# Kernel tuning notes

Hardware: AMD Instinct MI355X
Metric: run time of the kernel (lower is better)

Reference implementation:

```python
import jax, jax.numpy as jnp
import numpy as np

F_DIM = 256; H = 4; LAT = 256; BOT = 128
B = 64; NPG = 180; N = B * NPG; E = N * 16; HF = H * F_DIM
NEG_SLOPE = 0.2  # PyG GATConv default LeakyReLU slope


def _gat(x, src, dst, W, att_s, att_d, bias):
    # PyG GATConv (concat=True): h = x W, per-edge score LeakyReLU(a_s[src]+a_d[dst]),
    # softmax over incoming edges of each dst, weighted sum, concat heads, + bias.
    h = (x @ W).reshape(N, H, F_DIM)
    a_s = jnp.einsum('nhc,hc->nh', h, att_s)
    a_d = jnp.einsum('nhc,hc->nh', h, att_d)
    e = jax.nn.leaky_relu(a_s[src] + a_d[dst], NEG_SLOPE)          # [E+N, H]
    m = jax.ops.segment_max(e, dst, num_segments=N)                # stable softmax per dst
    p = jnp.exp(e - m[dst])
    s = jax.ops.segment_sum(p, dst, num_segments=N)
    alpha = p / (s[dst] + 1e-16)
    out = jax.ops.segment_sum(alpha[:, :, None] * h[src], dst, num_segments=N)
    return out.reshape(N, HF) + bias


def setup_inputs() -> dict:
    key = jax.random.key(0)
    ks = jax.random.split(key, 40)
    def rn(i, shape, scale):
        return jax.random.normal(ks[i], shape, jnp.float32) * jnp.float32(scale)
    inp = {}
    inp['z'] = jax.random.normal(ks[0], (B, LAT), jnp.float32)
    inp['condition'] = jax.random.normal(ks[1], (B, BOT), jnp.float32)
    dst = jax.random.randint(ks[2], (E,), 0, N)
    off = jax.random.randint(ks[3], (E,), 1, NPG)
    src = (dst + off) % N  # no self-loops by construction (PyG adds them itself)
    inp['edge_index'] = jnp.stack([src, dst]).astype(jnp.int32)
    inp['batch'] = jnp.repeat(jnp.arange(B, dtype=jnp.int32), NPG)
    def lin(i, fin, fout):
        s = 1.0 / np.sqrt(fin)
        return rn(i, (fin, fout), s), rn(i + 1, (fout,), s)
    inp['W_init'], inp['b_init'] = lin(4, LAT + BOT, F_DIM)
    inp['W1'] = rn(6, (F_DIM + 180, HF), 1.0 / np.sqrt(F_DIM + 180))
    inp['as1'] = rn(7, (H, F_DIM), 0.1); inp['ad1'] = rn(8, (H, F_DIM), 0.1)
    inp['b1'] = rn(9, (HF,), 0.1)
    inp['W2'] = rn(10, (HF, HF), 1.0 / np.sqrt(HF))
    inp['as2'] = rn(11, (H, F_DIM), 0.1); inp['ad2'] = rn(12, (H, F_DIM), 0.1)
    inp['b2'] = rn(13, (HF,), 0.1)
    inp['W3'] = rn(14, (HF, HF), 1.0 / np.sqrt(HF))
    inp['as3'] = rn(15, (H, F_DIM), 0.1); inp['ad3'] = rn(16, (H, F_DIM), 0.1)
    inp['b3'] = rn(17, (HF,), 0.1)
    inp['Wp'], inp['bp'] = lin(18, HF, F_DIM)
    inp['Wfp'], inp['bfp'] = lin(20, F_DIM, 2)
    inp['Ws'], inp['bs'] = lin(22, HF, F_DIM)
    inp['Wfs'], inp['bfs'] = lin(24, F_DIM, 2)
    inp['Wt'], inp['bt'] = lin(26, HF, F_DIM)
    inp['Wft'], inp['bft'] = lin(28, F_DIM, 1)
    return inp


def reference(z, condition, edge_index, batch, W_init, b_init,
              W1, as1, ad1, b1, W2, as2, ad2, b2, W3, as3, ad3, b3,
              Wp, bp, Wfp, bfp, Ws, bs, Wfs, bfs, Wt, bt, Wft, bft):
    zc = jnp.concatenate([z, condition], axis=1) @ W_init + b_init  # [B, F]
    x = zc[batch]                                                    # [N, F]
    # node order within each (sorted) batch segment -> one-hot(180)
    start = jnp.searchsorted(batch, jnp.arange(B, dtype=batch.dtype))
    order = jnp.arange(N) - start[batch]
    pos = jax.nn.one_hot(order, 180, dtype=x.dtype)
    x = jax.nn.relu(jnp.concatenate([x, pos], axis=1))               # [N, F+180]
    # add self loops (PyG GATConv default add_self_loops=True)
    loops = jnp.arange(N, dtype=edge_index.dtype)
    src = jnp.concatenate([edge_index[0], loops])
    dst = jnp.concatenate([edge_index[1], loops])
    x = jax.nn.relu(_gat(x, src, dst, W1, as1, ad1, b1))
    x = jax.nn.relu(_gat(x, src, dst, W2, as2, ad2, b2))
    x = jax.nn.relu(_gat(x, src, dst, W3, as3, ad3, b3))
    out_pos = jax.nn.relu(x @ Wp + bp) @ Wfp + bfp     # [N, 2]
    out_size = jax.nn.relu(x @ Ws + bs) @ Wfs + bfs    # [N, 2]
    out_theta = jax.nn.relu(x @ Wt + bt) @ Wft + bft   # [N, 1]
    return out_pos, out_size, out_theta
```

## Files before the change

kernel.cpp:

```cpp
#include <hip/hip_runtime.h>
#include <hip/hip_bf16.h>

#define NODES 11520
#define EDGES 184320
#define NB    64
#define NPG   180
#define CAP   64

typedef __bf16 bf16x8 __attribute__((ext_vector_type(8)));
typedef __bf16 bf16x4 __attribute__((ext_vector_type(4)));
typedef float  f32x4  __attribute__((ext_vector_type(4)));

__global__ __launch_bounds__(256) void k_init(
    const float* __restrict__ z, const float* __restrict__ cond,
    const float* __restrict__ Wi, const float* __restrict__ bi,
    const float* __restrict__ W1, float* __restrict__ Y1)
{
    __shared__ float xr[384];
    __shared__ float part[4][256];
    __shared__ float zr[256];
    const int b = blockIdx.x, t = threadIdx.x;
    xr[t] = (t < 256) ? z[b * 256 + t] : 0.f;
    if (t < 128) xr[256 + t] = cond[b * 128 + t];
    __syncthreads();
    {
        const int kq = t >> 6, tc = t & 63;
        f32x4 acc = {0.f, 0.f, 0.f, 0.f};
        const float* wbase = Wi + (size_t)(kq * 96) * 256 + 4 * tc;
        const float* xb = xr + kq * 96;
#pragma unroll 8
        for (int k = 0; k < 96; ++k) {
            const float4 w = *(const float4*)(wbase + (size_t)k * 256);
            const float x = xb[k];
            acc[0] = fmaf(x, w.x, acc[0]);
            acc[1] = fmaf(x, w.y, acc[1]);
            acc[2] = fmaf(x, w.z, acc[2]);
            acc[3] = fmaf(x, w.w, acc[3]);
        }
        *(f32x4*)&part[kq][4 * tc] = acc;
    }
    __syncthreads();
    zr[t] = fmaxf(bi[t] + part[0][t] + part[1][t] + part[2][t] + part[3][t], 0.f);
    __syncthreads();
    {
        f32x4 acc = {0.f, 0.f, 0.f, 0.f};
#pragma unroll 8
        for (int k = 0; k < 256; ++k) {
            const float4 w = *(const float4*)(W1 + (size_t)k * 1024 + 4 * t);
            const float x = zr[k];
            acc[0] = fmaf(x, w.x, acc[0]);
            acc[1] = fmaf(x, w.y, acc[1]);
            acc[2] = fmaf(x, w.z, acc[2]);
            acc[3] = fmaf(x, w.w, acc[3]);
        }
        *(f32x4*)(Y1 + (size_t)b * 1024 + 4 * t) = acc;
    }
}

__global__ __launch_bounds__(256) void k_h1(
    const float* __restrict__ Y1, const float* __restrict__ W1,
    const float* __restrict__ atts, const float* __restrict__ attd,
    __bf16* __restrict__ hb, float* __restrict__ asb, float* __restrict__ adb)
{
    const int n = blockIdx.x, t = threadIdx.x;
    const int g = n / NPG, o = n - g * NPG;
    const float4 y = *(const float4*)(Y1 + (size_t)g * 1024 + 4 * t);
    const float4 w = *(const float4*)(W1 + (size_t)(256 + o) * 1024 + 4 * t);
    const float4 h = {y.x + w.x, y.y + w.y, y.z + w.z, y.w + w.w};
    bf16x4 hv = {(__bf16)h.x, (__bf16)h.y, (__bf16)h.z, (__bf16)h.w};
    *(bf16x4*)(hb + (size_t)n * 1024 + 4 * t) = hv;
    const int head = t >> 6, c0 = (t & 63) * 4;
    const float4 s4 = *(const float4*)(atts + head * 256 + c0);
    const float4 d4 = *(const float4*)(attd + head * 256 + c0);
    float ps = h.x * s4.x + h.y * s4.y + h.z * s4.z + h.w * s4.w;
    float pd = h.x * d4.x + h.y * d4.y + h.z * d4.z + h.w * d4.w;
    for (int off = 32; off; off >>= 1) {
        ps += __shfl_xor(ps, off, 64);
        pd += __shfl_xor(pd, off, 64);
    }
    if ((t & 63) == 0) { asb[n * 4 + head] = ps; adb[n * 4 + head] = pd; }
}

__global__ __launch_bounds__(256) void k_hist(
    const int* __restrict__ ei, int* __restrict__ counts,
    int* __restrict__ bucket)
{
    const int e = blockIdx.x * 256 + threadIdx.x;
    if (e >= EDGES) return;
    const int s = ei[e], d = ei[EDGES + e];
    const int pos = atomicAdd(&counts[d], 1);
    if (pos < CAP) bucket[(size_t)d * CAP + pos] = s;
}

__global__ __launch_bounds__(256) void k_agg(
    const __bf16* __restrict__ hb, const float* __restrict__ asb,
    const float* __restrict__ adb, const int* __restrict__ counts,
    const int* __restrict__ bucket, const float* __restrict__ bias,
    __bf16* __restrict__ xout)
{
    const int l = blockIdx.x;
    const int n = (l & 7) * (NODES / 8) + (l >> 3);
    const int t = threadIdx.x;
    __shared__ float sc[CAP + 1][4];
    __shared__ int   ssrc[CAP + 1];
    __shared__ float sinv[4];
    const int deg = min(counts[n], CAP);
    const int ne  = deg + 1;
    if (t < deg)       ssrc[t] = bucket[(size_t)n * CAP + t];
    else if (t == deg) ssrc[t] = n;
    __syncthreads();
    if (t < ne) {
        const int s = ssrc[t];
        const float4 as4 = *(const float4*)(asb + (size_t)s * 4);
        const float4 ad4 = *(const float4*)(adb + (size_t)n * 4);
        const float v0 = as4.x + ad4.x, v1 = as4.y + ad4.y;
        const float v2 = as4.z + ad4.z, v3 = as4.w + ad4.w;
        sc[t][0] = v0 > 0.f ? v0 : 0.2f * v0;
        sc[t][1] = v1 > 0.f ? v1 : 0.2f * v1;
        sc[t][2] = v2 > 0.f ? v2 : 0.2f * v2;
        sc[t][3] = v3 > 0.f ? v3 : 0.2f * v3;
    }
    __syncthreads();
    const int wv = t >> 6, ln = t & 63;
    {
        float m = -1e30f;
        for (int k = ln; k < ne; k += 64) m = fmaxf(m, sc[k][wv]);
        for (int off = 32; off; off >>= 1) m = fmaxf(m, __shfl_xor(m, off, 64));
        float s = 0.f;
        for (int k = ln; k < ne; k += 64) {
            const float p = __expf(sc[k][wv] - m);
            sc[k][wv] = p;
            s += p;
        }
        for (int off = 32; off; off >>= 1) s += __shfl_xor(s, off, 64);
        if (ln == 0) sinv[wv] = 1.f / (s + 1e-16f);
    }
    __syncthreads();
    const int j0 = t * 4;
    const float inv = sinv[wv];
    float a0 = 0, a1 = 0, a2 = 0, a3 = 0;
    int k = 0;
    for (; k + 4 <= ne; k += 4) {
        float al[4]; bf16x4 hv[4];
#pragma unroll
        for (int u = 0; u < 4; ++u) {
            al[u] = sc[k + u][wv] * inv;
            hv[u] = *(const bf16x4*)(hb + (size_t)ssrc[k + u] * 1024 + j0);
        }
#pragma unroll
        for (int u = 0; u < 4; ++u) {
            a0 = fmaf(al[u], (float)hv[u][0], a0);
            a1 = fmaf(al[u], (float)hv[u][1], a1);
            a2 = fmaf(al[u], (float)hv[u][2], a2);
            a3 = fmaf(al[u], (float)hv[u][3], a3);
        }
    }
    for (; k < ne; ++k) {
        const float al = sc[k][wv] * inv;
        const bf16x4 hv = *(const bf16x4*)(hb + (size_t)ssrc[k] * 1024 + j0);
        a0 = fmaf(al, (float)hv[0], a0);
        a1 = fmaf(al, (float)hv[1], a1);
        a2 = fmaf(al, (float)hv[2], a2);
        a3 = fmaf(al, (float)hv[3], a3);
    }
    const float4 b4 = *(const float4*)(bias + j0);
    bf16x4 o = {(__bf16)fmaxf(a0 + b4.x, 0.f), (__bf16)fmaxf(a1 + b4.y, 0.f),
                (__bf16)fmaxf(a2 + b4.z, 0.f), (__bf16)fmaxf(a3 + b4.w, 0.f)};
    *(bf16x4*)(xout + (size_t)n * 1024 + j0) = o;
}

__global__ __launch_bounds__(256) void k_transW(
    const float* __restrict__ W2, const float* __restrict__ W3,
    __bf16* __restrict__ W2t, __bf16* __restrict__ W3t)
{
    const float* W = blockIdx.z ? W3 : W2;
    __bf16* WT = blockIdx.z ? W3t : W2t;
    __shared__ float t[32][33];
    const int n0 = blockIdx.x * 32, k0 = blockIdx.y * 32;
    const int tx = threadIdx.x & 31, ty = threadIdx.x >> 5;
#pragma unroll
    for (int i = 0; i < 32; i += 8)
        t[ty + i][tx] = W[(size_t)(k0 + ty + i) * 1024 + n0 + tx];
    __syncthreads();
#pragma unroll
    for (int i = 0; i < 32; i += 8)
        WT[(size_t)(n0 + ty + i) * 1024 + k0 + tx] = (__bf16)t[tx][ty + i];
}

__global__ __launch_bounds__(256) void k_transH(
    const float* __restrict__ Wp, const float* __restrict__ Ws,
    const float* __restrict__ Wt, __bf16* __restrict__ WHt,
    const float* __restrict__ bp, const float* __restrict__ bs,
    const float* __restrict__ bt, float* __restrict__ bc)
{
    if (blockIdx.x == 8) {
        if (blockIdx.y == 0) {
            const int t = blockIdx.z * 256 + threadIdx.x;
            const float v = blockIdx.z == 0 ? bp[threadIdx.x]
                          : blockIdx.z == 1 ? bs[threadIdx.x] : bt[threadIdx.x];
            bc[t] = v;
        }
        return;
    }
    const float* W = blockIdx.z == 0 ? Wp : blockIdx.z == 1 ? Ws : Wt;
    __bf16* WT = WHt + (size_t)blockIdx.z * 256 * 1024;
    __shared__ float t[32][33];
    const int n0 = blockIdx.x * 32, k0 = blockIdx.y * 32;
    const int tx = threadIdx.x & 31, ty = threadIdx.x >> 5;
#pragma unroll
    for (int i = 0; i < 32; i += 8)
        t[ty + i][tx] = W[(size_t)(k0 + ty + i) * 256 + n0 + tx];
    __syncthreads();
#pragma unroll
    for (int i = 0; i < 32; i += 8)
        WT[(size_t)(n0 + ty + i) * 1024 + k0 + tx] = (__bf16)t[tx][ty + i];
}

__global__ __launch_bounds__(256) void gemm_bf16_h(
    const __bf16* __restrict__ A,
    const __bf16* __restrict__ BT,
    __bf16* __restrict__ Cb,
    const float* __restrict__ atts, const float* __restrict__ attd,
    float* __restrict__ asb, float* __restrict__ adb,
    int M, int N, int K)
{
    const int lb = blockIdx.x;
    const int g = lb & 7, idx = lb >> 3;
    const int bx = idx & 7;
    const int by = (idx >> 3) * 8 + g;
    if (by * 128 >= M) return;
    const int m0 = by * 128, n0 = bx * 128;

    __shared__ __bf16 As[2 * 128 * 32];
    __shared__ __bf16 Bs[2 * 128 * 32];
    const int tid = threadIdx.x;
    const int w = tid >> 6, l = tid & 63;
    const int lr = l >> 2;
    const int lk = (l & 3) * 8;
    const int quad = l >> 4, r16 = l & 15;
    const int wm = (w >> 1) * 64, wn = (w & 1) * 64;

    f32x4 acc[4][4];
#pragma unroll
    for (int i = 0; i < 4; ++i)
#pragma unroll
        for (int j = 0; j < 4; ++j)
            acc[i][j] = (f32x4){0.f, 0.f, 0.f, 0.f};

    for (int k0 = 0; k0 < K; k0 += 64) {
#pragma unroll
        for (int h = 0; h < 2; ++h) {
#pragma unroll
            for (int cc = 0; cc < 2; ++cc) {
                const int c = 2 * w + cc;
                const int row = c * 16 + lr;
                __builtin_amdgcn_global_load_lds(
                    (const __attribute__((address_space(1))) void*)
                        (A + (size_t)(m0 + row) * K + k0 + h * 32 + lk),
                    (__attribute__((address_space(3))) void*)
                        (As + h * 4096 + c * 512),
                    16, 0, 0);
                __builtin_amdgcn_global_load_lds(
                    (const __attribute__((address_space(1))) void*)
                        (BT + (size_t)(n0 + row) * K + k0 + h * 32 + lk),
                    (__attribute__((address_space(3))) void*)
                        (Bs + h * 4096 + c * 512),
                    16, 0, 0);
            }
        }
        __syncthreads();
#pragma unroll
        for (int h = 0; h < 2; ++h) {
            bf16x8 af[4], bfr[4];
#pragma unroll
            for (int i = 0; i < 4; ++i)
                af[i] = *(const bf16x8*)(As + h * 4096 +
                                         (wm + i * 16 + r16) * 32 + quad * 8);
#pragma unroll
            for (int j = 0; j < 4; ++j)
                bfr[j] = *(const bf16x8*)(Bs + h * 4096 +
                                          (wn + j * 16 + r16) * 32 + quad * 8);
#pragma unroll
            for (int i = 0; i < 4; ++i)
#pragma unroll
                for (int j = 0; j < 4; ++j)
                    acc[i][j] = __builtin_amdgcn_mfma_f32_16x16x32_bf16(
                        af[i], bfr[j], acc[i][j], 0, 0, 0);
        }
        __syncthreads();
    }
    const int head = (n0 + wn) >> 8;
    const float* Sa = atts + head * 256;
    const float* Da = attd + head * 256;
#pragma unroll
    for (int i = 0; i < 4; ++i) {
#pragma unroll
        for (int r = 0; r < 4; ++r) {
            const int mg = m0 + wm + i * 16 + quad * 4 + r;
            float ps = 0.f, pd = 0.f;
#pragma unroll
            for (int j = 0; j < 4; ++j) {
                const int ng = n0 + wn + j * 16 + r16;
                const float v = acc[i][j][r];
                const int cl = ng & 255;
                ps = fmaf(v, Sa[cl], ps);
                pd = fmaf(v, Da[cl], pd);
                Cb[(size_t)mg * N + ng] = (__bf16)v;
            }
            for (int off = 8; off; off >>= 1) {
                ps += __shfl_xor(ps, off, 64);
                pd += __shfl_xor(pd, off, 64);
            }
            if (r16 == 0) {
                atomicAdd(&asb[mg * 4 + head], ps);
                atomicAdd(&adb[mg * 4 + head], pd);
            }
        }
    }
}

__global__ __launch_bounds__(256) void gemm_bf16_f32(
    const __bf16* __restrict__ A, const __bf16* __restrict__ BT,
    float* __restrict__ C, const float* __restrict__ bias,
    int M, int N, int K)
{
    const int lb = blockIdx.x;
    const int g = lb & 7, idx = lb >> 3;
    const int bx = idx % 6;
    const int by = (idx / 6) * 8 + g;
    if (by * 128 >= M) return;
    const int m0 = by * 128, n0 = bx * 128;

    __shared__ __bf16 As[2 * 128 * 32];
    __shared__ __bf16 Bs[2 * 128 * 32];
    const int tid = threadIdx.x;
    const int w = tid >> 6, l = tid & 63;
    const int lr = l >> 2;
    const int lk = (l & 3) * 8;
    const int quad = l >> 4, r16 = l & 15;
    const int wm = (w >> 1) * 64, wn = (w & 1) * 64;

    f32x4 acc[4][4];
#pragma unroll
    for (int i = 0; i < 4; ++i)
#pragma unroll
        for (int j = 0; j < 4; ++j)
            acc[i][j] = (f32x4){0.f, 0.f, 0.f, 0.f};

    for (int k0 = 0; k0 < K; k0 += 64) {
#pragma unroll
        for (int h = 0; h < 2; ++h) {
#pragma unroll
            for (int cc = 0; cc < 2; ++cc) {
                const int c = 2 * w + cc;
                const int row = c * 16 + lr;
                __builtin_amdgcn_global_load_lds(
                    (const __attribute__((address_space(1))) void*)
                        (A + (size_t)(m0 + row) * K + k0 + h * 32 + lk),
                    (__attribute__((address_space(3))) void*)
                        (As + h * 4096 + c * 512),
                    16, 0, 0);
                __builtin_amdgcn_global_load_lds(
                    (const __attribute__((address_space(1))) void*)
                        (BT + (size_t)(n0 + row) * K + k0 + h * 32 + lk),
                    (__attribute__((address_space(3))) void*)
                        (Bs + h * 4096 + c * 512),
                    16, 0, 0);
            }
        }
        __syncthreads();
#pragma unroll
        for (int h = 0; h < 2; ++h) {
            bf16x8 af[4], bfr[4];
#pragma unroll
            for (int i = 0; i < 4; ++i)
                af[i] = *(const bf16x8*)(As + h * 4096 +
                                         (wm + i * 16 + r16) * 32 + quad * 8);
#pragma unroll
            for (int j = 0; j < 4; ++j)
                bfr[j] = *(const bf16x8*)(Bs + h * 4096 +
                                          (wn + j * 16 + r16) * 32 + quad * 8);
#pragma unroll
            for (int i = 0; i < 4; ++i)
#pragma unroll
                for (int j = 0; j < 4; ++j)
                    acc[i][j] = __builtin_amdgcn_mfma_f32_16x16x32_bf16(
                        af[i], bfr[j], acc[i][j], 0, 0, 0);
        }
        __syncthreads();
    }
#pragma unroll
    for (int i = 0; i < 4; ++i) {
        const int mg = m0 + wm + i * 16 + quad * 4;
#pragma unroll
        for (int j = 0; j < 4; ++j) {
            const int ng = n0 + wn + j * 16 + r16;
            const float bz = bias[ng];
#pragma unroll
            for (int r = 0; r < 4; ++r)
                C[(size_t)(mg + r) * N + ng] = fmaxf(acc[i][j][r] + bz, 0.f);
        }
    }
}

__global__ __launch_bounds__(320) void k_final(
    const float* __restrict__ T,
    const float* __restrict__ Wfp, const float* __restrict__ bfp,
    const float* __restrict__ Wfs, const float* __restrict__ bfs,
    const float* __restrict__ Wft, const float* __restrict__ bft,
    float* __restrict__ out)
{
    const int n = blockIdx.x;
    const int w = threadIdx.x >> 6, l = threadIdx.x & 63;
    const float* trow;
    const float* Wf;
    float bv;
    int col, stride, oidx;
    if (w < 2) {
        trow = T + (size_t)n * 768;       Wf = Wfp; bv = bfp[w];
        col = w; stride = 2; oidx = 2 * n + w;
    } else if (w < 4) {
        trow = T + (size_t)n * 768 + 256; Wf = Wfs; bv = bfs[w - 2];
        col = w - 2; stride = 2; oidx = 2 * NODES + 2 * n + (w - 2);
    } else {
        trow = T + (size_t)n * 768 + 512; Wf = Wft; bv = bft[0];
        col = 0; stride = 1; oidx = 4 * NODES + n;
    }
    float s = 0.f;
    for (int c = l; c < 256; c += 64) s = fmaf(trow[c], Wf[c * stride + col], s);
    for (int off = 32; off; off >>= 1) s += __shfl_xor(s, off, 64);
    if (l == 0) out[oidx] = s + bv;
}

extern "C" void kernel_launch(void* const* d_in, const int* in_sizes, int n_in,
                              void* d_out, int out_size, void* d_ws, size_t ws_size,
                              hipStream_t stream)
{
    const float* z    = (const float*)d_in[0];
    const float* cond = (const float*)d_in[1];
    const int*   ei   = (const int*)  d_in[2];
    const float* Wi   = (const float*)d_in[4];
    const float* bi   = (const float*)d_in[5];
    const float* W1   = (const float*)d_in[6];
    const float* as1  = (const float*)d_in[7];
    const float* ad1  = (const float*)d_in[8];
    const float* b1   = (const float*)d_in[9];
    const float* W2   = (const float*)d_in[10];
    const float* as2  = (const float*)d_in[11];
    const float* ad2  = (const float*)d_in[12];
    const float* b2   = (const float*)d_in[13];
    const float* W3   = (const float*)d_in[14];
    const float* as3  = (const float*)d_in[15];
    const float* ad3  = (const float*)d_in[16];
    const float* b3   = (const float*)d_in[17];
    const float* Wp   = (const float*)d_in[18];
    const float* bp   = (const float*)d_in[19];
    const float* Wfp  = (const float*)d_in[20];
    const float* bfp  = (const float*)d_in[21];
    const float* Ws   = (const float*)d_in[22];
    const float* bs   = (const float*)d_in[23];
    const float* Wfs  = (const float*)d_in[24];
    const float* bfs  = (const float*)d_in[25];
    const float* Wt   = (const float*)d_in[26];
    const float* bt   = (const float*)d_in[27];
    const float* Wft  = (const float*)d_in[28];
    const float* bft  = (const float*)d_in[29];
    float* out = (float*)d_out;

    char* p = (char*)d_ws;
    __bf16* hb    = (__bf16*)p;           p += (size_t)NODES * 1024 * 2;
    __bf16* xb16  = (__bf16*)p;           p += (size_t)NODES * 1024 * 2;
    float* Tbuf   = (float*)p;            p += (size_t)NODES * 768 * 4;
    float* asb    = (float*)p;            p += (size_t)NODES * 4 * 4;
    float* adb    = (float*)p;            p += (size_t)NODES * 4 * 4;
    float* Y1     = (float*)p;            p += 64 * 1024 * 4;
    int*   counts = (int*)p;              p += (size_t)NODES * 4;
    int*   bucket = (int*)p;              p += (size_t)NODES * CAP * 4;
    __bf16* W2t   = (__bf16*)p;           p += (size_t)1024 * 1024 * 2;
    __bf16* W3t   = (__bf16*)p;           p += (size_t)1024 * 1024 * 2;
    __bf16* WHt   = (__bf16*)p;           p += (size_t)768 * 1024 * 2;
    float* biascat= (float*)p;            p += 768 * 4;

    k_transW<<<dim3(32, 32, 2), 256, 0, stream>>>(W2, W3, W2t, W3t);
    k_transH<<<dim3(9, 32, 3), 256, 0, stream>>>(Wp, Ws, Wt, WHt,
                                                 bp, bs, bt, biascat);

    hipMemsetAsync(counts, 0, NODES * sizeof(int), stream);
    k_hist<<<EDGES / 256, 256, 0, stream>>>(ei, counts, bucket);

    k_init<<<NB, 256, 0, stream>>>(z, cond, Wi, bi, W1, Y1);
    k_h1<<<NODES, 256, 0, stream>>>(Y1, W1, as1, ad1, hb, asb, adb);
    k_agg<<<NODES, 256, 0, stream>>>(hb, asb, adb, counts, bucket, b1, xb16);

    hipMemsetAsync(asb, 0, (size_t)NODES * 8 * sizeof(float), stream);
    gemm_bf16_h<<<8 * 96, 256, 0, stream>>>(xb16, W2t, hb, as2, ad2,
                                            asb, adb, NODES, 1024, 1024);
    k_agg<<<NODES, 256, 0, stream>>>(hb, asb, adb, counts, bucket, b2, xb16);

    hipMemsetAsync(asb, 0, (size_t)NODES * 8 * sizeof(float), stream);
    gemm_bf16_h<<<8 * 96, 256, 0, stream>>>(xb16, W3t, hb, as3, ad3,
                                            asb, adb, NODES, 1024, 1024);
    k_agg<<<NODES, 256, 0, stream>>>(hb, asb, adb, counts, bucket, b3, xb16);

    gemm_bf16_f32<<<6 * 96, 256, 0, stream>>>(xb16, WHt, Tbuf, biascat,
                                              NODES, 768, 1024);
    k_final<<<NODES, 320, 0, stream>>>(Tbuf, Wfp, bfp, Wfs, bfs, Wft, bft, out);
}
```

Before: 445.3 us.

## Double-buffer GEMM, fuse head MLP epilogue, pack two nodes per agg block

```diff
diff --git a/kernel.cpp b/kernel.cpp
--- a/kernel.cpp
+++ b/kernel.cpp
@@ -60,9 +60,12 @@
 __global__ __launch_bounds__(256) void k_h1(
     const float* __restrict__ Y1, const float* __restrict__ W1,
     const float* __restrict__ atts, const float* __restrict__ attd,
-    __bf16* __restrict__ hb, float* __restrict__ asb, float* __restrict__ adb)
+    __bf16* __restrict__ hb, float* __restrict__ asb, float* __restrict__ adb,
+    float* __restrict__ zas, float* __restrict__ zad)
 {
     const int n = blockIdx.x, t = threadIdx.x;
+    if (t < 4)      zas[n * 4 + t] = 0.f;
+    else if (t < 8) zad[n * 4 + (t - 4)] = 0.f;
     const int g = n / NPG, o = n - g * NPG;
     const float4 y = *(const float4*)(Y1 + (size_t)g * 1024 + 4 * t);
     const float4 w = *(const float4*)(W1 + (size_t)(256 + o) * 1024 + 4 * t);
@@ -96,77 +99,90 @@
     const __bf16* __restrict__ hb, const float* __restrict__ asb,
     const float* __restrict__ adb, const int* __restrict__ counts,
     const int* __restrict__ bucket, const float* __restrict__ bias,
-    __bf16* __restrict__ xout)
-{
-    const int l = blockIdx.x;
-    const int n = (l & 7) * (NODES / 8) + (l >> 3);
+    __bf16* __restrict__ xout, float* __restrict__ zas, float* __restrict__ zad)
+{
+    const int b = blockIdx.x;
+    const int nb = (b & 7) * (NODES / 8) + 2 * (b >> 3);
     const int t = threadIdx.x;
-    __shared__ float sc[CAP + 1][4];
-    __shared__ int   ssrc[CAP + 1];
-    __shared__ float sinv[4];
+    const int half = t >> 7, tt = t & 127;
+    const int n = nb + half;
+    __shared__ float sc[2][CAP + 1][4];
+    __shared__ int   ssrc[2][CAP + 1];
+    __shared__ float sinv[2][4];
+    if (zas != nullptr) {
+        if (t < 8)       zas[nb * 4 + t] = 0.f;
+        else if (t < 16) zad[nb * 4 + (t - 8)] = 0.f;
+    }
     const int deg = min(counts[n], CAP);
     const int ne  = deg + 1;
-    if (t < deg)       ssrc[t] = bucket[(size_t)n * CAP + t];
-    else if (t == deg) ssrc[t] = n;
-    __syncthreads();
-    if (t < ne) {
-        const int s = ssrc[t];
+    if (tt < deg)       ssrc[half][tt] = bucket[(size_t)n * CAP + tt];
+    else if (tt == deg) ssrc[half][tt] = n;
+    __syncthreads();
+    if (tt < ne) {
+        const int s = ssrc[half][tt];
         const float4 as4 = *(const float4*)(asb + (size_t)s * 4);
         const float4 ad4 = *(const float4*)(adb + (size_t)n * 4);
         const float v0 = as4.x + ad4.x, v1 = as4.y + ad4.y;
         const float v2 = as4.z + ad4.z, v3 = as4.w + ad4.w;
-        sc[t][0] = v0 > 0.f ? v0 : 0.2f * v0;
-        sc[t][1] = v1 > 0.f ? v1 : 0.2f * v1;
-        sc[t][2] = v2 > 0.f ? v2 : 0.2f * v2;
-        sc[t][3] = v3 > 0.f ? v3 : 0.2f * v3;
-    }
-    __syncthreads();
-    const int wv = t >> 6, ln = t & 63;
-    {
+        sc[half][tt][0] = v0 > 0.f ? v0 : 0.2f * v0;
+        sc[half][tt][1] = v1 > 0.f ? v1 : 0.2f * v1;
+        sc[half][tt][2] = v2 > 0.f ? v2 : 0.2f * v2;
+        sc[half][tt][3] = v3 > 0.f ? v3 : 0.2f * v3;
+    }
+    __syncthreads();
+    const int ln = t & 63, hw = (t >> 6) & 1;
+#pragma unroll
+    for (int hh = 0; hh < 2; ++hh) {
+        const int head = hw * 2 + hh;
         float m = -1e30f;
-        for (int k = ln; k < ne; k += 64) m = fmaxf(m, sc[k][wv]);
+        for (int k = ln; k < ne; k += 64) m = fmaxf(m, sc[half][k][head]);
         for (int off = 32; off; off >>= 1) m = fmaxf(m, __shfl_xor(m, off, 64));
         float s = 0.f;
         for (int k = ln; k < ne; k += 64) {
-            const float p = __expf(sc[k][wv] - m);
-            sc[k][wv] = p;
+            const float p = __expf(sc[half][k][head] - m);
+            sc[half][k][head] = p;
             s += p;
         }
         for (int off = 32; off; off >>= 1) s += __shfl_xor(s, off, 64);
-        if (ln == 0) sinv[wv] = 1.f / (s + 1e-16f);
-    }
-    __syncthreads();
-    const int j0 = t * 4;
-    const float inv = sinv[wv];
-    float a0 = 0, a1 = 0, a2 = 0, a3 = 0;
+        if (ln == 0) sinv[half][head] = 1.f / (s + 1e-16f);
+    }
+    __syncthreads();
+    const int j0 = tt * 8, hd = tt >> 5;
+    const float inv = sinv[half][hd];
+    float a[8] = {0, 0, 0, 0, 0, 0, 0, 0};
     int k = 0;
     for (; k + 4 <= ne; k += 4) {
-        float al[4]; bf16x4 hv[4];
+        float al[4]; bf16x8 hv[4];
 #pragma unroll
         for (int u = 0; u < 4; ++u) {
-            al[u] = sc[k + u][wv] * inv;
-            hv[u] = *(const bf16x4*)(hb + (size_t)ssrc[k + u] * 1024 + j0);
-        }
-#pragma unroll
-        for (int u = 0; u < 4; ++u) {
-            a0 = fmaf(al[u], (float)hv[u][0], a0);
-            a1 = fmaf(al[u], (float)hv[u][1], a1);
-            a2 = fmaf(al[u], (float)hv[u][2], a2);
-            a3 = fmaf(al[u], (float)hv[u][3], a3);
-        }
+            al[u] = sc[half][k + u][hd] * inv;
+            hv[u] = *(const bf16x8*)(hb + (size_t)ssrc[half][k + u] * 1024 + j0);
+        }
+#pragma unroll
+        for (int u = 0; u < 4; ++u)
+#pragma unroll
+            for (int e = 0; e < 8; ++e)
+                a[e] = fmaf(al[u], (float)hv[u][e], a[e]);
     }
     for (; k < ne; ++k) {
-        const float al = sc[k][wv] * inv;
-        const bf16x4 hv = *(const bf16x4*)(hb + (size_t)ssrc[k] * 1024 + j0);
-        a0 = fmaf(al, (float)hv[0], a0);
-        a1 = fmaf(al, (float)hv[1], a1);
-        a2 = fmaf(al, (float)hv[2], a2);
-        a3 = fmaf(al, (float)hv[3], a3);
-    }
-    const float4 b4 = *(const float4*)(bias + j0);
-    bf16x4 o = {(__bf16)fmaxf(a0 + b4.x, 0.f), (__bf16)fmaxf(a1 + b4.y, 0.f),
-                (__bf16)fmaxf(a2 + b4.z, 0.f), (__bf16)fmaxf(a3 + b4.w, 0.f)};
-    *(bf16x4*)(xout + (size_t)n * 1024 + j0) = o;
+        const float al = sc[half][k][hd] * inv;
+        const bf16x8 hv = *(const bf16x8*)(hb + (size_t)ssrc[half][k] * 1024 + j0);
+#pragma unroll
+        for (int e = 0; e < 8; ++e)
+            a[e] = fmaf(al, (float)hv[e], a[e]);
+    }
+    const float4 b4a = *(const float4*)(bias + j0);
+    const float4 b4b = *(const float4*)(bias + j0 + 4);
+    bf16x8 o;
+    o[0] = (__bf16)fmaxf(a[0] + b4a.x, 0.f);
+    o[1] = (__bf16)fmaxf(a[1] + b4a.y, 0.f);
+    o[2] = (__bf16)fmaxf(a[2] + b4a.z, 0.f);
+    o[3] = (__bf16)fmaxf(a[3] + b4a.w, 0.f);
+    o[4] = (__bf16)fmaxf(a[4] + b4b.x, 0.f);
+    o[5] = (__bf16)fmaxf(a[5] + b4b.y, 0.f);
+    o[6] = (__bf16)fmaxf(a[6] + b4b.z, 0.f);
+    o[7] = (__bf16)fmaxf(a[7] + b4b.w, 0.f);
+    *(bf16x8*)(xout + (size_t)n * 1024 + j0) = o;
 }
 
 __global__ __launch_bounds__(256) void k_transW(
@@ -216,9 +232,70 @@
         WT[(size_t)(n0 + ty + i) * 1024 + k0 + tx] = (__bf16)t[tx][ty + i];
 }
 
+#define STAGE(buf, kbase)                                                      \
+    {                                                                          \
+        _Pragma("unroll")                                                      \
+        for (int h = 0; h < 2; ++h) {                                          \
+            _Pragma("unroll")                                                  \
+            for (int cc = 0; cc < 2; ++cc) {                                   \
+                const int c = 2 * w + cc;                                      \
+                const int row = c * 16 + lr;                                   \
+                __builtin_amdgcn_global_load_lds(                              \
+                    (const __attribute__((address_space(1))) void*)            \
+                        (A + (size_t)(m0 + row) * K + (kbase) + h * 32 + lk),  \
+                    (__attribute__((address_space(3))) void*)                  \
+                        (As + (buf) * 8192 + h * 4096 + c * 512), 16, 0, 0);   \
+                __builtin_amdgcn_global_load_lds(                              \
+                    (const __attribute__((address_space(1))) void*)            \
+                        (BT + (size_t)(n0 + row) * K + (kbase) + h * 32 + lk), \
+                    (__attribute__((address_space(3))) void*)                  \
+                        (Bs + (buf) * 8192 + h * 4096 + c * 512), 16, 0, 0);   \
+            }                                                                  \
+        }                                                                      \
+    }
+
+#define COMPUTE(buf)                                                           \
+    {                                                                          \
+        _Pragma("unroll")                                                      \
+        for (int h = 0; h < 2; ++h) {                                          \
+            bf16x8 af[4], bfr[4];                                              \
+            _Pragma("unroll")                                                  \
+            for (int i = 0; i < 4; ++i)                                        \
+                af[i] = *(const bf16x8*)(As + (buf) * 8192 + h * 4096 +        \
+                                         (wm + i * 16 + r16) * 32 + quad * 8); \
+            _Pragma("unroll")                                                  \
+            for (int j = 0; j < 4; ++j)                                        \
+                bfr[j] = *(const bf16x8*)(Bs + (buf) * 8192 + h * 4096 +       \
+                                          (wn + j * 16 + r16) * 32 + quad * 8);\
+            _Pragma("unroll")                                                  \
+            for (int i = 0; i < 4; ++i)                                        \
+                _Pragma("unroll")                                              \
+                for (int j = 0; j < 4; ++j)                                    \
+                    acc[i][j] = __builtin_amdgcn_mfma_f32_16x16x32_bf16(       \
+                        af[i], bfr[j], acc[i][j], 0, 0, 0);                    \
+        }                                                                      \
+    }
+
+#define GEMM_MAINLOOP()                                                        \
+    f32x4 acc[4][4];                                                           \
+    _Pragma("unroll")                                                          \
+    for (int i = 0; i < 4; ++i)                                                \
+        _Pragma("unroll")                                                      \
+        for (int j = 0; j < 4; ++j)                                            \
+            acc[i][j] = (f32x4){0.f, 0.f, 0.f, 0.f};                           \
+    STAGE(0, 0);                                                               \
+    int cur = 0;                                                               \
+    for (int k0 = 64; k0 < K; k0 += 64) {                                      \
+        __syncthreads();                                                       \
+        STAGE(cur ^ 1, k0);                                                    \
+        COMPUTE(cur);                                                          \
+        cur ^= 1;                                                              \
+    }                                                                          \
+    __syncthreads();                                                           \
+    COMPUTE(cur);
+
 __global__ __launch_bounds__(256) void gemm_bf16_h(
-    const __bf16* __restrict__ A,
-    const __bf16* __restrict__ BT,
+    const __bf16* __restrict__ A, const __bf16* __restrict__ BT,
     __bf16* __restrict__ Cb,
     const float* __restrict__ atts, const float* __restrict__ attd,
     float* __restrict__ asb, float* __restrict__ adb,
@@ -231,67 +308,24 @@
     if (by * 128 >= M) return;
     const int m0 = by * 128, n0 = bx * 128;
 
-    __shared__ __bf16 As[2 * 128 * 32];
-    __shared__ __bf16 Bs[2 * 128 * 32];
+    __shared__ __bf16 As[2 * 128 * 64];
+    __shared__ __bf16 Bs[2 * 128 * 64];
     const int tid = threadIdx.x;
     const int w = tid >> 6, l = tid & 63;
-    const int lr = l >> 2;
-    const int lk = (l & 3) * 8;
+    const int lr = l >> 2, lk = (l & 3) * 8;
     const int quad = l >> 4, r16 = l & 15;
     const int wm = (w >> 1) * 64, wn = (w & 1) * 64;
 
-    f32x4 acc[4][4];
-#pragma unroll
-    for (int i = 0; i < 4; ++i)
-#pragma unroll
-        for (int j = 0; j < 4; ++j)
-            acc[i][j] = (f32x4){0.f, 0.f, 0.f, 0.f};
-
-    for (int k0 = 0; k0 < K; k0 += 64) {
-#pragma unroll
-        for (int h = 0; h < 2; ++h) {
-#pragma unroll
-            for (int cc = 0; cc < 2; ++cc) {
-                const int c = 2 * w + cc;
-                const int row = c * 16 + lr;
-                __builtin_amdgcn_global_load_lds(
-                    (const __attribute__((address_space(1))) void*)
-                        (A + (size_t)(m0 + row) * K + k0 + h * 32 + lk),
-                    (__attribute__((address_space(3))) void*)
-                        (As + h * 4096 + c * 512),
-                    16, 0, 0);
-                __builtin_amdgcn_global_load_lds(
-                    (const __attribute__((address_space(1))) void*)
-                        (BT + (size_t)(n0 + row) * K + k0 + h * 32 + lk),
-                    (__attribute__((address_space(3))) void*)
-                        (Bs + h * 4096 + c * 512),
-                    16, 0, 0);
-            }
-        }
-        __syncthreads();
-#pragma unroll
-        for (int h = 0; h < 2; ++h) {
-            bf16x8 af[4], bfr[4];
-#pragma unroll
-            for (int i = 0; i < 4; ++i)
-                af[i] = *(const bf16x8*)(As + h * 4096 +
-                                         (wm + i * 16 + r16) * 32 + quad * 8);
-#pragma unroll
-            for (int j = 0; j < 4; ++j)
-                bfr[j] = *(const bf16x8*)(Bs + h * 4096 +
-                                          (wn + j * 16 + r16) * 32 + quad * 8);
-#pragma unroll
-            for (int i = 0; i < 4; ++i)
-#pragma unroll
-                for (int j = 0; j < 4; ++j)
-                    acc[i][j] = __builtin_amdgcn_mfma_f32_16x16x32_bf16(
-                        af[i], bfr[j], acc[i][j], 0, 0, 0);
-        }
-        __syncthreads();
-    }
+    GEMM_MAINLOOP();
+
     const int head = (n0 + wn) >> 8;
-    const float* Sa = atts + head * 256;
-    const float* Da = attd + head * 256;
+    float sa[4], da[4];
+#pragma unroll
+    for (int j = 0; j < 4; ++j) {
+        const int cl = (n0 + wn + j * 16 + r16) & 255;
+        sa[j] = atts[head * 256 + cl];
+        da[j] = attd[head * 256 + cl];
+    }
 #pragma unroll
     for (int i = 0; i < 4; ++i) {
 #pragma unroll
@@ -302,9 +336,8 @@
             for (int j = 0; j < 4; ++j) {
                 const int ng = n0 + wn + j * 16 + r16;
                 const float v = acc[i][j][r];
-                const int cl = ng & 255;
-                ps = fmaf(v, Sa[cl], ps);
-                pd = fmaf(v, Da[cl], pd);
+                ps = fmaf(v, sa[j], ps);
+                pd = fmaf(v, da[j], pd);
                 Cb[(size_t)mg * N + ng] = (__bf16)v;
             }
             for (int off = 8; off; off >>= 1) {
@@ -319,10 +352,13 @@
     }
 }
 
-__global__ __launch_bounds__(256) void gemm_bf16_f32(
+__global__ __launch_bounds__(256) void gemm_heads(
     const __bf16* __restrict__ A, const __bf16* __restrict__ BT,
-    float* __restrict__ C, const float* __restrict__ bias,
-    int M, int N, int K)
+    const float* __restrict__ biascat,
+    const float* __restrict__ Wfp, const float* __restrict__ bfp,
+    const float* __restrict__ Wfs, const float* __restrict__ bfs,
+    const float* __restrict__ Wft, const float* __restrict__ bft,
+    float* __restrict__ out, int M, int K)
 {
     const int lb = blockIdx.x;
     const int g = lb & 7, idx = lb >> 3;
@@ -331,105 +367,57 @@
     if (by * 128 >= M) return;
     const int m0 = by * 128, n0 = bx * 128;
 
-    __shared__ __bf16 As[2 * 128 * 32];
-    __shared__ __bf16 Bs[2 * 128 * 32];
+    __shared__ __bf16 As[2 * 128 * 64];
+    __shared__ __bf16 Bs[2 * 128 * 64];
     const int tid = threadIdx.x;
     const int w = tid >> 6, l = tid & 63;
-    const int lr = l >> 2;
-    const int lk = (l & 3) * 8;
+    const int lr = l >> 2, lk = (l & 3) * 8;
     const int quad = l >> 4, r16 = l & 15;
     const int wm = (w >> 1) * 64, wn = (w & 1) * 64;
 
-    f32x4 acc[4][4];
-#pragma unroll
-    for (int i = 0; i < 4; ++i)
-#pragma unroll
-        for (int j = 0; j < 4; ++j)
-            acc[i][j] = (f32x4){0.f, 0.f, 0.f, 0.f};
-
-    for (int k0 = 0; k0 < K; k0 += 64) {
-#pragma unroll
-        for (int h = 0; h < 2; ++h) {
-#pragma unroll
-            for (int cc = 0; cc < 2; ++cc) {
-                const int c = 2 * w + cc;
-                const int row = c * 16 + lr;
-                __builtin_amdgcn_global_load_lds(
-                    (const __attribute__((address_space(1))) void*)
-                        (A + (size_t)(m0 + row) * K + k0 + h * 32 + lk),
-                    (__attribute__((address_space(3))) void*)
-                        (As + h * 4096 + c * 512),
-                    16, 0, 0);
-                __builtin_amdgcn_global_load_lds(
-                    (const __attribute__((address_space(1))) void*)
-                        (BT + (size_t)(n0 + row) * K + k0 + h * 32 + lk),
-                    (__attribute__((address_space(3))) void*)
-                        (Bs + h * 4096 + c * 512),
-                    16, 0, 0);
-            }
-        }
-        __syncthreads();
-#pragma unroll
-        for (int h = 0; h < 2; ++h) {
-            bf16x8 af[4], bfr[4];
-#pragma unroll
-            for (int i = 0; i < 4; ++i)
-                af[i] = *(const bf16x8*)(As + h * 4096 +
-                                         (wm + i * 16 + r16) * 32 + quad * 8);
-#pragma unroll
-            for (int j = 0; j < 4; ++j)
-                bfr[j] = *(const bf16x8*)(Bs + h * 4096 +
-                                          (wn + j * 16 + r16) * 32 + quad * 8);
-#pragma unroll
-            for (int i = 0; i < 4; ++i)
-#pragma unroll
-                for (int j = 0; j < 4; ++j)
-                    acc[i][j] = __builtin_amdgcn_mfma_f32_16x16x32_bf16(
-                        af[i], bfr[j], acc[i][j], 0, 0, 0);
-        }
-        __syncthreads();
-    }
+    GEMM_MAINLOOP();
+
+    const int hg = bx >> 1;
+    const float* Wf = hg == 0 ? Wfp : hg == 1 ? Wfs : Wft;
+    const int nout = hg == 2 ? 1 : 2;
+    float wf0[4], wf1[4], bz[4];
+#pragma unroll
+    for (int j = 0; j < 4; ++j) {
+        const int ng = n0 + wn + j * 16 + r16;
+        const int cl = ng & 255;
+        bz[j]  = biascat[ng];
+        wf0[j] = Wf[cl * nout];
+        wf1[j] = nout == 2 ? Wf[cl * nout + 1] : 0.f;
+    }
+    const bool addb = ((bx & 1) == 0) && (wn == 0);
+    const float fb0 = hg == 0 ? bfp[0] : hg == 1 ? bfs[0] : bft[0];
+    const float fb1 = hg == 2 ? 0.f : (hg == 0 ? bfp[1] : bfs[1]);
 #pragma unroll
     for (int i = 0; i < 4; ++i) {
-        const int mg = m0 + wm + i * 16 + quad * 4;
-#pragma unroll
-        for (int j = 0; j < 4; ++j) {
-            const int ng = n0 + wn + j * 16 + r16;
-            const float bz = bias[ng];
-#pragma unroll
-            for (int r = 0; r < 4; ++r)
-                C[(size_t)(mg + r) * N + ng] = fmaxf(acc[i][j][r] + bz, 0.f);
-        }
-    }
-}
-
-__global__ __launch_bounds__(320) void k_final(
-    const float* __restrict__ T,
-    const float* __restrict__ Wfp, const float* __restrict__ bfp,
-    const float* __restrict__ Wfs, const float* __restrict__ bfs,
-    const float* __restrict__ Wft, const float* __restrict__ bft,
-    float* __restrict__ out)
-{
-    const int n = blockIdx.x;
-    const int w = threadIdx.x >> 6, l = threadIdx.x & 63;
-    const float* trow;
-    const float* Wf;
-    float bv;
-    int col, stride, oidx;
-    if (w < 2) {
-        trow = T + (size_t)n * 768;       Wf = Wfp; bv = bfp[w];
-        col = w; stride = 2; oidx = 2 * n + w;
-    } else if (w < 4) {
-        trow = T + (size_t)n * 768 + 256; Wf = Wfs; bv = bfs[w - 2];
-        col = w - 2; stride = 2; oidx = 2 * NODES + 2 * n + (w - 2);
-    } else {
-        trow = T + (size_t)n * 768 + 512; Wf = Wft; bv = bft[0];
-        col = 0; stride = 1; oidx = 4 * NODES + n;
-    }
-    float s = 0.f;
-    for (int c = l; c < 256; c += 64) s = fmaf(trow[c], Wf[c * stride + col], s);
-    for (int off = 32; off; off >>= 1) s += __shfl_xor(s, off, 64);
-    if (l == 0) out[oidx] = s + bv;
+#pragma unroll
+        for (int r = 0; r < 4; ++r) {
+            const int mg = m0 + wm + i * 16 + quad * 4 + r;
+            float o0 = 0.f, o1 = 0.f;
+#pragma unroll
+            for (int j = 0; j < 4; ++j) {
+                const float v = fmaxf(acc[i][j][r] + bz[j], 0.f);
+                o0 = fmaf(v, wf0[j], o0);
+                o1 = fmaf(v, wf1[j], o1);
+            }
+            for (int off = 8; off; off >>= 1) {
+                o0 += __shfl_xor(o0, off, 64);
+                o1 += __shfl_xor(o1, off, 64);
+            }
+            if (r16 == 0) {
+                if (addb) { o0 += fb0; o1 += fb1; }
+                const size_t base = hg == 0 ? 2 * (size_t)mg
+                                 : hg == 1 ? 2 * (size_t)NODES + 2 * (size_t)mg
+                                 : 4 * (size_t)NODES + (size_t)mg;
+                atomicAdd(&out[base], o0);
+                if (nout == 2) atomicAdd(&out[base + 1], o1);
+            }
+        }
+    }
 }
 
 extern "C" void kernel_launch(void* const* d_in, const int* in_sizes, int n_in,
@@ -470,9 +458,10 @@
     char* p = (char*)d_ws;
     __bf16* hb    = (__bf16*)p;           p += (size_t)NODES * 1024 * 2;
     __bf16* xb16  = (__bf16*)p;           p += (size_t)NODES * 1024 * 2;
-    float* Tbuf   = (float*)p;            p += (size_t)NODES * 768 * 4;
-    float* asb    = (float*)p;            p += (size_t)NODES * 4 * 4;
-    float* adb    = (float*)p;            p += (size_t)NODES * 4 * 4;
+    float* asA    = (float*)p;            p += (size_t)NODES * 4 * 4;
+    float* adA    = (float*)p;            p += (size_t)NODES * 4 * 4;
+    float* asB    = (float*)p;            p += (size_t)NODES * 4 * 4;
+    float* adB    = (float*)p;            p += (size_t)NODES * 4 * 4;
     float* Y1     = (float*)p;            p += 64 * 1024 * 4;
     int*   counts = (int*)p;              p += (size_t)NODES * 4;
     int*   bucket = (int*)p;              p += (size_t)NODES * CAP * 4;
@@ -481,28 +470,29 @@
     __bf16* WHt   = (__bf16*)p;           p += (size_t)768 * 1024 * 2;
     float* biascat= (float*)p;            p += 768 * 4;
 
+    hipMemsetAsync(out, 0, (size_t)out_size * sizeof(float), stream);
+    hipMemsetAsync(counts, 0, NODES * sizeof(int), stream);
+
     k_transW<<<dim3(32, 32, 2), 256, 0, stream>>>(W2, W3, W2t, W3t);
     k_transH<<<dim3(9, 32, 3), 256, 0, stream>>>(Wp, Ws, Wt, WHt,
                                                  bp, bs, bt, biascat);
-
-    hipMemsetAsync(counts, 0, NODES * sizeof(int), stream);
     k_hist<<<EDGES / 256, 256, 0, stream>>>(ei, counts, bucket);
 
     k_init<<<NB, 256, 0, stream>>>(z, cond, Wi, bi, W1, Y1);
-    k_h1<<<NODES, 256, 0, stream>>>(Y1, W1, as1, ad1, hb, asb, adb);
-    k_agg<<<NODES, 256, 0, stream>>>(hb, asb, adb, counts, bucket, b1, xb16);
-
-    hipMemsetAsync(asb, 0, (size_t)NODES * 8 * sizeof(float), stream);
+    k_h1<<<NODES, 256, 0, stream>>>(Y1, W1, as1, ad1, hb, asA, adA, asB, adB);
+    k_agg<<<NODES / 2, 256, 0, stream>>>(hb, asA, adA, counts, bucket, b1,
+                                         xb16, nullptr, nullptr);
+
     gemm_bf16_h<<<8 * 96, 256, 0, stream>>>(xb16, W2t, hb, as2, ad2,
-                                            asb, adb, NODES, 1024, 1024);
-    k_agg<<<NODES, 256, 0, stream>>>(hb, asb, adb, counts, bucket, b2, xb16);
-
-    hipMemsetAsync(asb, 0, (size_t)NODES * 8 * sizeof(float), stream);
+                                            asB, adB, NODES, 1024, 1024);
+    k_agg<<<NODES / 2, 256, 0, stream>>>(hb, asB, adB, counts, bucket, b2,
+                                         xb16, asA, adA);
     gemm_bf16_h<<<8 * 96, 256, 0, stream>>>(xb16, W3t, hb, as3, ad3,
-                                            asb, adb, NODES, 1024, 1024);
-    k_agg<<<NODES, 256, 0, stream>>>(hb, asb, adb, counts, bucket, b3, xb16);
-
-    gemm_bf16_f32<<<6 * 96, 256, 0, stream>>>(xb16, WHt, Tbuf, biascat,
-                                              NODES, 768, 1024);
-    k_final<<<NODES, 320, 0, stream>>>(Tbuf, Wfp, bfp, Wfs, bfs, Wft, bft, out);
-}
+                                            asA, adA, NODES, 1024, 1024);
+    k_agg<<<NODES / 2, 256, 0, stream>>>(hb, asA, adA, counts, bucket, b3,
+                                         xb16, nullptr, nullptr);
+
+    gemm_heads<<<6 * 96, 256, 0, stream>>>(xb16, WHt, biascat,
+                                           Wfp, bfp, Wfs, bfs, Wft, bft,
+                                           out, NODES, 1024);
+}
```

New measurement: 431.8 us. 1.03x faster.
